# Performance work log

Measured on AMD Instinct MI355X. Metric: run time of the kernel, lower is better.

The kernel has to match this reference:

```python
import jax, jax.numpy as jnp
import numpy as np

B, S, E, H, WIN = 2, 2048, 2048, 16, 256
HD = E // H


def setup_inputs() -> dict:
    key = jax.random.key(0)
    ks = jax.random.split(key, 20)
    def w(k, i, o):
        return jax.random.normal(k, (i, o), jnp.float32) * (1.0 / np.sqrt(i))
    return {
        'x': jax.random.normal(ks[0], (B, S, E), jnp.float32),
        'global_attention_mask': jax.random.randint(ks[1], (B, S), 0, 2, jnp.int32),
        'Wq': w(ks[2], E, E), 'bq': jnp.zeros((E,), jnp.float32),
        'Wk': w(ks[3], E, E), 'bk': jnp.zeros((E,), jnp.float32),
        'Wv': w(ks[4], E, E), 'bv': jnp.zeros((E,), jnp.float32),
        'Wlq': w(ks[5], E, E), 'blq': jnp.zeros((E,), jnp.float32),
        'Wlk': w(ks[6], E, E), 'blk': jnp.zeros((E,), jnp.float32),
        'Wlv': w(ks[7], E, E), 'blv': jnp.zeros((E,), jnp.float32),
        'Wp': w(ks[8], E, E), 'bp': jnp.zeros((E,), jnp.float32),
    }


def reference(x, global_attention_mask, Wq, bq, Wk, bk, Wv, bv,
              Wlq, blq, Wlk, blk, Wlv, blv, Wp, bp):
    b, s, e = x.shape
    h, hd, win = H, HD, WIN
    scale = 1.0 / np.sqrt(hd)

    # ---- global attention (flash_attn_func, non-causal, alibi slopes = 1.0 per head) ----
    q = (x @ Wq + bq).reshape(b, s, h, hd)
    k = (x @ Wk + bk).reshape(b, s, h, hd)
    v = (x @ Wv + bv).reshape(b, s, h, hd)
    idx = jnp.arange(s)
    alibi = -jnp.abs(idx[:, None] - idx[None, :]).astype(x.dtype)  # slope 1.0, same for all heads
    scores = jnp.einsum('bqhd,bkhd->bhqk', q, k) * scale + alibi  # [b,h,s,s]
    ctx_g = jnp.einsum('bhqk,bkhd->bqhd', jax.nn.softmax(scores, axis=-1), v).reshape(b, s, e)

    # ---- local chunked-window attention ----
    pad = (-s) % win
    sp = s + pad
    nch = sp // win
    def proj_pad(Wm, bm):
        y = x @ Wm + bm
        return jnp.pad(y, ((0, 0), (0, pad), (0, 0))).reshape(b, nch, win, h, hd)
    lq = proj_pad(Wlq, blq)
    lk = proj_pad(Wlk, blk)
    lv = proj_pad(Wlv, blv)
    sc = jnp.einsum('bcqhd,bckhd->bchqk', lq, lk) * scale
    valid = (jnp.arange(sp) < s).reshape(nch, win)  # mask padded keys
    sc = jnp.where(valid[None, :, None, None, :], sc, jnp.asarray(-1e9, sc.dtype))
    ctx_l = jnp.einsum('bchqk,bckhd->bcqhd', jax.nn.softmax(sc, axis=-1), lv)
    ctx_l = ctx_l.reshape(b, sp, e)[:, :s]

    # ---- mix global/local per token via mask, then output projection ----
    m = (global_attention_mask == 1)[:, :, None]  # [b,s,1]
    ctx = jnp.where(m, ctx_g, ctx_l)
    return ctx @ Wp + bp
```

## Files before the change

kernel.cpp:

```cpp
#include <hip/hip_runtime.h>

typedef unsigned short u16;
typedef unsigned int u32;
typedef __bf16 bf16x8 __attribute__((ext_vector_type(8)));
typedef float f32x4 __attribute__((ext_vector_type(4)));

#define NB 2
#define SS 2048
#define EE 2048
#define HH 16
#define HDIM 128
#define WINLEN 256
#define SCALEF 0.08838834764831845f
#define LOG2E 1.4426950408889634f

__device__ __forceinline__ u16 f2bf(float f) {
  u32 u = __builtin_bit_cast(u32, f);
  u32 r = (u + 0x7FFFu + ((u >> 16) & 1u)) >> 16;
  return (u16)r;
}

__device__ __forceinline__ void gld_lds16(const void* g, void* l) {
  __builtin_amdgcn_global_load_lds((const __attribute__((address_space(1))) u32*)g,
                                   (__attribute__((address_space(3))) u32*)l, 16, 0, 0);
}

__global__ __launch_bounds__(256) void cast_x(const float* __restrict__ x, u16* __restrict__ xb) {
  const int i = blockIdx.x * 256 + threadIdx.x;
  float4 v = ((const float4*)x)[i];
  uint2 o;
  o.x = (u32)f2bf(v.x) | ((u32)f2bf(v.y) << 16);
  o.y = (u32)f2bf(v.z) | ((u32)f2bf(v.w) << 16);
  ((uint2*)xb)[i] = o;
}

__global__ __launch_bounds__(256) void tcast(const float* __restrict__ W, u16* __restrict__ Wt) {
  __shared__ float t[32][33];
  const int n0 = blockIdx.x * 32, k0 = blockIdx.y * 32;
  const int tx = threadIdx.x & 31, ty = threadIdx.x >> 5;
#pragma unroll
  for (int i = ty; i < 32; i += 8)
    t[i][tx] = W[(size_t)(k0 + i) * EE + n0 + tx];
  __syncthreads();
#pragma unroll
  for (int i = ty; i < 32; i += 8)
    Wt[(size_t)(n0 + i) * EE + k0 + tx] = f2bf(t[tx][i]);
}

__global__ __launch_bounds__(256) void vtrans(const u16* __restrict__ V, u16* __restrict__ Vt) {
  __shared__ u16 t[32][33];
  const int s0 = blockIdx.x * 32, d0 = blockIdx.y * 32;
  const int bh = blockIdx.z;
  const int b = bh >> 4, h = bh & 15;
  const int tx = threadIdx.x & 31, ty = threadIdx.x >> 5;
  const u16* src = V + ((size_t)b * SS) * EE + h * HDIM;
#pragma unroll
  for (int i = ty; i < 32; i += 8)
    t[i][tx] = src[(size_t)(s0 + i) * EE + d0 + tx];
  __syncthreads();
  u16* dst = Vt + (size_t)bh * HDIM * SS;
#pragma unroll
  for (int i = ty; i < 32; i += 8)
    dst[(size_t)(d0 + i) * SS + s0 + tx] = t[tx][i];
}

__global__ __launch_bounds__(256) void gemm_bt(
    const u16* __restrict__ A, const u16* __restrict__ Bt,
    const float* __restrict__ bias, u16* __restrict__ Cb, float* __restrict__ Cf) {
  __shared__ u16 As[128 * 32];
  __shared__ u16 Bs[128 * 32];
  const int tid = threadIdx.x;
  const int lane = tid & 63;
  const int wv = tid >> 6;
  const int wr = wv >> 1, wc = wv & 1;
  const int fr = lane & 15, fg = lane >> 4;
  const int m0 = blockIdx.x * 128, n0 = blockIdx.y * 128;
  const int srow = tid >> 2;
  const int scol = (tid & 3) * 8;
  f32x4 acc[4][4] = {};
  const u16* pa0 = A + (size_t)(m0 + srow) * 2048 + scol;
  const u16* pa1 = A + (size_t)(m0 + 64 + srow) * 2048 + scol;
  const u16* pb0 = Bt + (size_t)(n0 + srow) * 2048 + scol;
  const u16* pb1 = Bt + (size_t)(n0 + 64 + srow) * 2048 + scol;
  for (int k0 = 0; k0 < 2048; k0 += 32) {
    gld_lds16(pa0 + k0, As + tid * 8);
    gld_lds16(pa1 + k0, As + 2048 + tid * 8);
    gld_lds16(pb0 + k0, Bs + tid * 8);
    gld_lds16(pb1 + k0, Bs + 2048 + tid * 8);
    __syncthreads();
    bf16x8 af[4], bfg[4];
#pragma unroll
    for (int m = 0; m < 4; ++m)
      af[m] = *(const bf16x8*)(As + (wr * 64 + m * 16 + fr) * 32 + fg * 8);
#pragma unroll
    for (int n = 0; n < 4; ++n)
      bfg[n] = *(const bf16x8*)(Bs + (wc * 64 + n * 16 + fr) * 32 + fg * 8);
#pragma unroll
    for (int m = 0; m < 4; ++m)
#pragma unroll
      for (int n = 0; n < 4; ++n)
        acc[m][n] = __builtin_amdgcn_mfma_f32_16x16x32_bf16(af[m], bfg[n], acc[m][n], 0, 0, 0);
    __syncthreads();
  }
#pragma unroll
  for (int m = 0; m < 4; ++m) {
    const int gr0 = m0 + wr * 64 + m * 16 + fg * 4;
#pragma unroll
    for (int n = 0; n < 4; ++n) {
      const int gc = n0 + wc * 64 + n * 16 + fr;
      const float bv = bias[gc];
#pragma unroll
      for (int j = 0; j < 4; ++j) {
        float v = acc[m][n][j] + bv;
        size_t off = (size_t)(gr0 + j) * 2048 + gc;
        if (Cf) Cf[off] = v;
        else Cb[off] = f2bf(v);
      }
    }
  }
}

template <bool LOCAL>
__global__ __launch_bounds__(256) void attn_kernel(
    const u16* __restrict__ Q, const u16* __restrict__ K,
    const u16* __restrict__ Vt, u16* __restrict__ O) {
  __shared__ u16 Pt[4][32 * 32];
  const int tid = threadIdx.x;
  const int lane = tid & 63;
  const int wv = tid >> 6;
  const int fr = lane & 15, fg = lane >> 4;
  const int qbase = blockIdx.x * 128;
  const int bh = blockIdx.y;
  const int b = bh >> 4, h = bh & 15;
  const int qw = qbase + wv * 32;
  const size_t rowbase = (size_t)b * SS;

  bf16x8 qf[2][4];
#pragma unroll
  for (int m = 0; m < 2; ++m)
#pragma unroll
    for (int ds = 0; ds < 4; ++ds)
      qf[m][ds] = *(const bf16x8*)(Q + (rowbase + qw + m * 16 + fr) * EE + h * HDIM + ds * 32 + fg * 8);

  f32x4 acc[2][8] = {};
  float mrun[2][4], lrun[2][4];
#pragma unroll
  for (int m = 0; m < 2; ++m)
#pragma unroll
    for (int j = 0; j < 4; ++j) { mrun[m][j] = -1e30f; lrun[m][j] = 0.f; }

  int lo, hi;
  if (LOCAL) {
    lo = (qbase >> 8) * (WINLEN / 32);
    hi = lo + (WINLEN / 32) - 1;
  } else {
    lo = (qw - 160) >> 5; if (lo < 0) lo = 0;
    hi = (qw + 191) >> 5; if (hi > SS / 32 - 1) hi = SS / 32 - 1;
  }

  for (int kti = lo; kti <= hi; ++kti) {
    const int kt = kti * 32;
    f32x4 sf[2][2] = {};
#pragma unroll
    for (int ds = 0; ds < 4; ++ds) {
      bf16x8 kf[2];
#pragma unroll
      for (int n = 0; n < 2; ++n)
        kf[n] = *(const bf16x8*)(K + (rowbase + kt + n * 16 + fr) * EE + h * HDIM + ds * 32 + fg * 8);
#pragma unroll
      for (int m = 0; m < 2; ++m)
#pragma unroll
        for (int n = 0; n < 2; ++n)
          sf[m][n] = __builtin_amdgcn_mfma_f32_16x16x32_bf16(qf[m][ds], kf[n], sf[m][n], 0, 0, 0);
    }
    float p[2][2][4];
#pragma unroll
    for (int m = 0; m < 2; ++m) {
      float rmax[4];
#pragma unroll
      for (int j = 0; j < 4; ++j) {
        float s0 = sf[m][0][j] * SCALEF;
        float s1 = sf[m][1][j] * SCALEF;
        if (!LOCAL) {
          const float qr = (float)(qw + m * 16 + fg * 4 + j);
          s0 -= fabsf(qr - (float)(kt + fr));
          s1 -= fabsf(qr - (float)(kt + 16 + fr));
        }
        p[m][0][j] = s0;
        p[m][1][j] = s1;
        float r = fmaxf(s0, s1);
#pragma unroll
        for (int xm = 1; xm < 16; xm <<= 1)
          r = fmaxf(r, __shfl_xor(r, xm));
        rmax[j] = r;
      }
#pragma unroll
      for (int j = 0; j < 4; ++j) {
        const float mold = mrun[m][j];
        const float mnew = fmaxf(mold, rmax[j]);
        const float corr = exp2f((mold - mnew) * LOG2E);
        mrun[m][j] = mnew;
        const float p0 = exp2f((p[m][0][j] - mnew) * LOG2E);
        const float p1 = exp2f((p[m][1][j] - mnew) * LOG2E);
        p[m][0][j] = p0;
        p[m][1][j] = p1;
        float rs = p0 + p1;
#pragma unroll
        for (int xm = 1; xm < 16; xm <<= 1)
          rs += __shfl_xor(rs, xm);
        lrun[m][j] = lrun[m][j] * corr + rs;
#pragma unroll
        for (int n = 0; n < 8; ++n) acc[m][n][j] *= corr;
      }
#pragma unroll
      for (int n = 0; n < 2; ++n)
#pragma unroll
        for (int j = 0; j < 4; ++j)
          Pt[wv][(m * 16 + fg * 4 + j) * 32 + n * 16 + fr] = f2bf(p[m][n][j]);
    }
    asm volatile("s_waitcnt lgkmcnt(0)" ::: "memory");
    bf16x8 ap[2];
#pragma unroll
    for (int m = 0; m < 2; ++m)
      ap[m] = *(const bf16x8*)(&Pt[wv][(m * 16 + fr) * 32 + fg * 8]);
#pragma unroll
    for (int n = 0; n < 8; ++n) {
      const bf16x8 vf = *(const bf16x8*)(Vt + ((size_t)bh * HDIM + n * 16 + fr) * SS + kt + fg * 8);
#pragma unroll
      for (int m = 0; m < 2; ++m)
        acc[m][n] = __builtin_amdgcn_mfma_f32_16x16x32_bf16(ap[m], vf, acc[m][n], 0, 0, 0);
    }
  }
#pragma unroll
  for (int m = 0; m < 2; ++m)
#pragma unroll
    for (int n = 0; n < 8; ++n)
#pragma unroll
      for (int j = 0; j < 4; ++j) {
        const int qr = qw + m * 16 + fg * 4 + j;
        const float v = acc[m][n][j] / lrun[m][j];
        O[(rowbase + qr) * EE + h * HDIM + n * 16 + fr] = f2bf(v);
      }
}

__global__ __launch_bounds__(256) void mix_kernel(
    const u16* __restrict__ cg, const u16* __restrict__ cl,
    const int* __restrict__ mask, u16* __restrict__ ctx) {
  const size_t i = (size_t)blockIdx.x * 256 + threadIdx.x;
  const size_t base = i * 8;
  const int row = (int)(base >> 11);
  const u16* src = (mask[row] == 1) ? cg : cl;
  *(uint4*)(ctx + base) = *(const uint4*)(src + base);
}

extern "C" void kernel_launch(void* const* d_in, const int* in_sizes, int n_in,
                              void* d_out, int out_size, void* d_ws, size_t ws_size,
                              hipStream_t stream) {
  (void)in_sizes; (void)n_in; (void)out_size; (void)ws_size;
  const float* x = (const float*)d_in[0];
  const int* gmask = (const int*)d_in[1];
  const float* Wq = (const float*)d_in[2];   const float* bq = (const float*)d_in[3];
  const float* Wk = (const float*)d_in[4];   const float* bk = (const float*)d_in[5];
  const float* Wv = (const float*)d_in[6];   const float* bv = (const float*)d_in[7];
  const float* Wlq = (const float*)d_in[8];  const float* blq = (const float*)d_in[9];
  const float* Wlk = (const float*)d_in[10]; const float* blk = (const float*)d_in[11];
  const float* Wlv = (const float*)d_in[12]; const float* blv = (const float*)d_in[13];
  const float* Wp = (const float*)d_in[14];  const float* bp = (const float*)d_in[15];
  float* out = (float*)d_out;

  char* w = (char*)d_ws;
  u16* xb   = (u16*)(w + (size_t)0);
  u16* wt   = (u16*)(w + ((size_t)16 << 20));
  u16* qB   = (u16*)(w + ((size_t)24 << 20));
  u16* kB   = (u16*)(w + ((size_t)40 << 20));
  u16* vB   = (u16*)(w + ((size_t)56 << 20));
  u16* lqB  = (u16*)(w + ((size_t)72 << 20));
  u16* lkB  = (u16*)(w + ((size_t)88 << 20));
  u16* lvB  = (u16*)(w + ((size_t)104 << 20));
  u16* vtB  = (u16*)(w + ((size_t)120 << 20));
  u16* lvtB = (u16*)(w + ((size_t)136 << 20));
  u16* cgB  = (u16*)(w + ((size_t)152 << 20));
  u16* clB  = (u16*)(w + ((size_t)168 << 20));

  cast_x<<<8192, 256, 0, stream>>>(x, xb);

  const float* Ws[6] = {Wq, Wk, Wv, Wlq, Wlk, Wlv};
  const float* bs[6] = {bq, bk, bv, blq, blk, blv};
  u16* outs[6] = {qB, kB, vB, lqB, lkB, lvB};
  for (int i = 0; i < 6; ++i) {
    tcast<<<dim3(64, 64), 256, 0, stream>>>(Ws[i], wt);
    gemm_bt<<<dim3(32, 16), 256, 0, stream>>>(xb, wt, bs[i], outs[i], nullptr);
  }

  vtrans<<<dim3(64, 4, 32), 256, 0, stream>>>(vB, vtB);
  vtrans<<<dim3(64, 4, 32), 256, 0, stream>>>(lvB, lvtB);

  attn_kernel<false><<<dim3(16, 32), 256, 0, stream>>>(qB, kB, vtB, cgB);
  attn_kernel<true><<<dim3(16, 32), 256, 0, stream>>>(lqB, lkB, lvtB, clB);

  mix_kernel<<<4096, 256, 0, stream>>>(cgB, clB, gmask, xb);

  tcast<<<dim3(64, 64), 256, 0, stream>>>(Wp, wt);
  gemm_bt<<<dim3(32, 16), 256, 0, stream>>>(xb, wt, bp, nullptr, out);
}
```

Before: 722.1 us.

## Batch six projection GEMMs, stage attention K/V through LDS, swizzle block order

Converts all six input weight matrices in one launch and runs the six projections as a single wide GEMM with concatenated bias, writing each output into its own plane. Attention now double-buffers K and V tiles in XOR-swizzled shared memory, replacing per-wave global loads, and uses a fixed eight-tile key range. Softmax scale and log2e are folded into one multiply. Both the GEMM and attention remap workgroup IDs for cache locality, and attention writes its output in place over Q. The aim is fewer launches, better reuse and fewer redundant global reads, at the cost of more LDS per block and a fixed window assumption.

Measured after the change: 664.1 us. 1.09x faster.

```diff
diff --git a/kernel.cpp b/kernel.cpp
--- a/kernel.cpp
+++ b/kernel.cpp
@@ -34,10 +34,9 @@
   ((uint2*)xb)[i] = o;
 }
 
-__global__ __launch_bounds__(256) void tcast(const float* __restrict__ W, u16* __restrict__ Wt) {
+__device__ __forceinline__ void tcast_body(const float* __restrict__ W, u16* __restrict__ Wt,
+                                           int n0, int k0, int tx, int ty) {
   __shared__ float t[32][33];
-  const int n0 = blockIdx.x * 32, k0 = blockIdx.y * 32;
-  const int tx = threadIdx.x & 31, ty = threadIdx.x >> 5;
 #pragma unroll
   for (int i = ty; i < 32; i += 8)
     t[i][tx] = W[(size_t)(k0 + i) * EE + n0 + tx];
@@ -45,6 +44,19 @@
 #pragma unroll
   for (int i = ty; i < 32; i += 8)
     Wt[(size_t)(n0 + i) * EE + k0 + tx] = f2bf(t[tx][i]);
+}
+
+__global__ __launch_bounds__(256) void tcast(const float* __restrict__ W, u16* __restrict__ Wt) {
+  tcast_body(W, Wt, blockIdx.x * 32, blockIdx.y * 32, threadIdx.x & 31, threadIdx.x >> 5);
+}
+
+__global__ __launch_bounds__(256) void tcast6(
+    const float* __restrict__ W0, const float* __restrict__ W1, const float* __restrict__ W2,
+    const float* __restrict__ W3, const float* __restrict__ W4, const float* __restrict__ W5,
+    u16* __restrict__ dst) {
+  const float* Ws[6] = {W0, W1, W2, W3, W4, W5};
+  tcast_body(Ws[blockIdx.z], dst + (size_t)blockIdx.z * EE * EE,
+             blockIdx.x * 32, blockIdx.y * 32, threadIdx.x & 31, threadIdx.x >> 5);
 }
 
 __global__ __launch_bounds__(256) void vtrans(const u16* __restrict__ V, u16* __restrict__ Vt) {
@@ -64,9 +76,10 @@
     dst[(size_t)(d0 + i) * SS + s0 + tx] = t[tx][i];
 }
 
+template <int MODE>
 __global__ __launch_bounds__(256) void gemm_bt(
     const u16* __restrict__ A, const u16* __restrict__ Bt,
-    const float* __restrict__ bias, u16* __restrict__ Cb, float* __restrict__ Cf) {
+    const float* __restrict__ bias, void* __restrict__ Cout) {
   __shared__ u16 As[128 * 32];
   __shared__ u16 Bs[128 * 32];
   const int tid = threadIdx.x;
@@ -74,7 +87,10 @@
   const int wv = tid >> 6;
   const int wr = wv >> 1, wc = wv & 1;
   const int fr = lane & 15, fg = lane >> 4;
-  const int m0 = blockIdx.x * 128, n0 = blockIdx.y * 128;
+  int lin = blockIdx.y * gridDim.x + blockIdx.x;
+  const int nwg = gridDim.x * gridDim.y;
+  lin = (lin & 7) * (nwg >> 3) + (lin >> 3);
+  const int m0 = (lin % gridDim.x) * 128, n0 = (lin / gridDim.x) * 128;
   const int srow = tid >> 2;
   const int scol = (tid & 3) * 8;
   f32x4 acc[4][4] = {};
@@ -112,9 +128,12 @@
 #pragma unroll
       for (int j = 0; j < 4; ++j) {
         float v = acc[m][n][j] + bv;
-        size_t off = (size_t)(gr0 + j) * 2048 + gc;
-        if (Cf) Cf[off] = v;
-        else Cb[off] = f2bf(v);
+        if (MODE == 0) {
+          size_t off = ((size_t)(gc >> 11) << 23) + (size_t)(gr0 + j) * 2048 + (gc & 2047);
+          ((u16*)Cout)[off] = f2bf(v);
+        } else {
+          ((float*)Cout)[(size_t)(gr0 + j) * 2048 + gc] = v;
+        }
       }
     }
   }
@@ -124,16 +143,28 @@
 __global__ __launch_bounds__(256) void attn_kernel(
     const u16* __restrict__ Q, const u16* __restrict__ K,
     const u16* __restrict__ Vt, u16* __restrict__ O) {
+  __shared__ u16 Ks[2][32 * 128];
+  __shared__ u16 Vs[2][128 * 32];
   __shared__ u16 Pt[4][32 * 32];
   const int tid = threadIdx.x;
   const int lane = tid & 63;
   const int wv = tid >> 6;
   const int fr = lane & 15, fg = lane >> 4;
-  const int qbase = blockIdx.x * 128;
-  const int bh = blockIdx.y;
+  int lin = blockIdx.y * 16 + blockIdx.x;
+  lin = (lin & 7) * 64 + (lin >> 3);
+  const int qbase = (lin & 15) * 128;
+  const int bh = lin >> 4;
   const int b = bh >> 4, h = bh & 15;
   const int qw = qbase + wv * 32;
   const size_t rowbase = (size_t)b * SS;
+  int kstart;
+  if (LOCAL) {
+    kstart = qbase & ~255;
+  } else {
+    kstart = qbase - 64;
+    if (kstart < 0) kstart = 0;
+    if (kstart > SS - 256) kstart = SS - 256;
+  }
 
   bf16x8 qf[2][4];
 #pragma unroll
@@ -149,24 +180,43 @@
 #pragma unroll
     for (int j = 0; j < 4; ++j) { mrun[m][j] = -1e30f; lrun[m][j] = 0.f; }
 
-  int lo, hi;
-  if (LOCAL) {
-    lo = (qbase >> 8) * (WINLEN / 32);
-    hi = lo + (WINLEN / 32) - 1;
-  } else {
-    lo = (qw - 160) >> 5; if (lo < 0) lo = 0;
-    hi = (qw + 191) >> 5; if (hi > SS / 32 - 1) hi = SS / 32 - 1;
-  }
-
-  for (int kti = lo; kti <= hi; ++kti) {
-    const int kt = kti * 32;
+  const u16* Kg = K + (rowbase + kstart) * EE + h * HDIM;
+  const u16* Vg = Vt + (size_t)bh * HDIM * SS + kstart;
+  const int r0 = tid >> 4;
+  const int kslot = (tid & 15) ^ (r0 & 7);
+  const int d0 = tid >> 2;
+  const int vslot = (tid & 3) ^ ((tid >> 3) & 3);
+
+  auto STAGE = [&](int buf, int t) {
+    const u16* kg = Kg + (size_t)t * 32 * EE;
+    gld_lds16(kg + (size_t)r0 * EE + kslot * 8, &Ks[buf][0] + tid * 8);
+    gld_lds16(kg + (size_t)(16 + r0) * EE + kslot * 8, &Ks[buf][2048] + tid * 8);
+    const u16* vg = Vg + t * 32;
+    gld_lds16(vg + (size_t)d0 * SS + vslot * 8, &Vs[buf][0] + tid * 8);
+    gld_lds16(vg + (size_t)(64 + d0) * SS + vslot * 8, &Vs[buf][2048] + tid * 8);
+  };
+
+  const float C1 = SCALEF * LOG2E;
+
+  STAGE(0, 0);
+  for (int t = 0; t < 8; ++t) {
+    const int buf = t & 1;
+    if (t < 7) {
+      STAGE(buf ^ 1, t + 1);
+      asm volatile("s_waitcnt vmcnt(4)" ::: "memory");
+    } else {
+      asm volatile("s_waitcnt vmcnt(0)" ::: "memory");
+    }
+    __builtin_amdgcn_s_barrier();
+
+    const int kt = kstart + t * 32;
     f32x4 sf[2][2] = {};
 #pragma unroll
     for (int ds = 0; ds < 4; ++ds) {
       bf16x8 kf[2];
 #pragma unroll
       for (int n = 0; n < 2; ++n)
-        kf[n] = *(const bf16x8*)(K + (rowbase + kt + n * 16 + fr) * EE + h * HDIM + ds * 32 + fg * 8);
+        kf[n] = *(const bf16x8*)(&Ks[buf][(n * 16 + fr) * 128 + ((ds * 32 + fg * 8) ^ ((fr & 7) * 8))]);
 #pragma unroll
       for (int m = 0; m < 2; ++m)
 #pragma unroll
@@ -179,12 +229,12 @@
       float rmax[4];
 #pragma unroll
       for (int j = 0; j < 4; ++j) {
-        float s0 = sf[m][0][j] * SCALEF;
-        float s1 = sf[m][1][j] * SCALEF;
+        float s0 = sf[m][0][j] * C1;
+        float s1 = sf[m][1][j] * C1;
         if (!LOCAL) {
           const float qr = (float)(qw + m * 16 + fg * 4 + j);
-          s0 -= fabsf(qr - (float)(kt + fr));
-          s1 -= fabsf(qr - (float)(kt + 16 + fr));
+          s0 -= fabsf(qr - (float)(kt + fr)) * LOG2E;
+          s1 -= fabsf(qr - (float)(kt + 16 + fr)) * LOG2E;
         }
         p[m][0][j] = s0;
         p[m][1][j] = s1;
@@ -198,10 +248,10 @@
       for (int j = 0; j < 4; ++j) {
         const float mold = mrun[m][j];
         const float mnew = fmaxf(mold, rmax[j]);
-        const float corr = exp2f((mold - mnew) * LOG2E);
+        const float corr = exp2f(mold - mnew);
         mrun[m][j] = mnew;
-        const float p0 = exp2f((p[m][0][j] - mnew) * LOG2E);
-        const float p1 = exp2f((p[m][1][j] - mnew) * LOG2E);
+        const float p0 = exp2f(p[m][0][j] - mnew);
+        const float p1 = exp2f(p[m][1][j] - mnew);
         p[m][0][j] = p0;
         p[m][1][j] = p1;
         float rs = p0 + p1;
@@ -225,11 +275,12 @@
       ap[m] = *(const bf16x8*)(&Pt[wv][(m * 16 + fr) * 32 + fg * 8]);
 #pragma unroll
     for (int n = 0; n < 8; ++n) {
-      const bf16x8 vf = *(const bf16x8*)(Vt + ((size_t)bh * HDIM + n * 16 + fr) * SS + kt + fg * 8);
+      const bf16x8 vf = *(const bf16x8*)(&Vs[buf][(n * 16 + fr) * 32 + ((fg * 8) ^ (((fr >> 1) & 3) * 8))]);
 #pragma unroll
       for (int m = 0; m < 2; ++m)
         acc[m][n] = __builtin_amdgcn_mfma_f32_16x16x32_bf16(ap[m], vf, acc[m][n], 0, 0, 0);
     }
+    __builtin_amdgcn_s_barrier();
   }
 #pragma unroll
   for (int m = 0; m < 2; ++m)
@@ -269,37 +320,37 @@
   float* out = (float*)d_out;
 
   char* w = (char*)d_ws;
-  u16* xb   = (u16*)(w + (size_t)0);
-  u16* wt   = (u16*)(w + ((size_t)16 << 20));
-  u16* qB   = (u16*)(w + ((size_t)24 << 20));
-  u16* kB   = (u16*)(w + ((size_t)40 << 20));
-  u16* vB   = (u16*)(w + ((size_t)56 << 20));
-  u16* lqB  = (u16*)(w + ((size_t)72 << 20));
-  u16* lkB  = (u16*)(w + ((size_t)88 << 20));
-  u16* lvB  = (u16*)(w + ((size_t)104 << 20));
-  u16* vtB  = (u16*)(w + ((size_t)120 << 20));
-  u16* lvtB = (u16*)(w + ((size_t)136 << 20));
-  u16* cgB  = (u16*)(w + ((size_t)152 << 20));
-  u16* clB  = (u16*)(w + ((size_t)168 << 20));
+  u16* xb    = (u16*)(w);
+  u16* WtAll = (u16*)(w + ((size_t)16 << 20));
+  u16* wtP   = (u16*)(w + ((size_t)16 << 20));
+  u16* vtB   = (u16*)(w + ((size_t)32 << 20));
+  u16* lvtB  = (u16*)(w + ((size_t)48 << 20));
+  u16* projout = (u16*)(w + ((size_t)64 << 20));
+  u16* qB  = projout;
+  u16* kB  = projout + ((size_t)1 << 23);
+  u16* vB  = projout + ((size_t)2 << 23);
+  u16* lqB = projout + ((size_t)3 << 23);
+  u16* lkB = projout + ((size_t)4 << 23);
+  u16* lvB = projout + ((size_t)5 << 23);
+  float* biasAll = (float*)(w + ((size_t)160 << 20));
 
   cast_x<<<8192, 256, 0, stream>>>(x, xb);
-
-  const float* Ws[6] = {Wq, Wk, Wv, Wlq, Wlk, Wlv};
+  tcast6<<<dim3(64, 64, 6), 256, 0, stream>>>(Wq, Wk, Wv, Wlq, Wlk, Wlv, WtAll);
   const float* bs[6] = {bq, bk, bv, blq, blk, blv};
-  u16* outs[6] = {qB, kB, vB, lqB, lkB, lvB};
-  for (int i = 0; i < 6; ++i) {
-    tcast<<<dim3(64, 64), 256, 0, stream>>>(Ws[i], wt);
-    gemm_bt<<<dim3(32, 16), 256, 0, stream>>>(xb, wt, bs[i], outs[i], nullptr);
-  }
+  for (int i = 0; i < 6; ++i)
+    hipMemcpyAsync(biasAll + i * 2048, bs[i], 2048 * sizeof(float),
+                   hipMemcpyDeviceToDevice, stream);
+
+  gemm_bt<0><<<dim3(32, 96), 256, 0, stream>>>(xb, WtAll, biasAll, projout);
 
   vtrans<<<dim3(64, 4, 32), 256, 0, stream>>>(vB, vtB);
   vtrans<<<dim3(64, 4, 32), 256, 0, stream>>>(lvB, lvtB);
 
-  attn_kernel<false><<<dim3(16, 32), 256, 0, stream>>>(qB, kB, vtB, cgB);
-  attn_kernel<true><<<dim3(16, 32), 256, 0, stream>>>(lqB, lkB, lvtB, clB);
-
-  mix_kernel<<<4096, 256, 0, stream>>>(cgB, clB, gmask, xb);
-
-  tcast<<<dim3(64, 64), 256, 0, stream>>>(Wp, wt);
-  gemm_bt<<<dim3(32, 16), 256, 0, stream>>>(xb, wt, bp, nullptr, out);
-}
+  attn_kernel<false><<<dim3(16, 32), 256, 0, stream>>>(qB, kB, vtB, qB);
+  attn_kernel<true><<<dim3(16, 32), 256, 0, stream>>>(lqB, lkB, lvtB, lqB);
+
+  mix_kernel<<<4096, 256, 0, stream>>>(qB, lqB, gmask, xb);
+
+  tcast<<<dim3(64, 64), 256, 0, stream>>>(Wp, wtP);
+  gemm_bt<1><<<dim3(32, 16), 256, 0, stream>>>(xb, wtP, bp, out);
+}
```
